# Optimization experiments

Measured on AMD Instinct MI355X. Metric: run time of the kernel, lower is better.

The kernel has to match this reference:

```python
import jax, jax.numpy as jnp
import numpy as np

C = 32
H = 8

def _layernorm(x, scale, bias, eps=1e-5):
    mu = jnp.mean(x, axis=-1, keepdims=True)
    var = jnp.mean(jnp.square(x - mu), axis=-1, keepdims=True)
    return (x - mu) * jax.lax.rsqrt(var + eps) * scale + bias


def setup_inputs() -> dict:
    key = jax.random.key(0)
    ks = jax.random.split(key, 10)
    B, s, i, j = 1, 128, 256, 256
    m = jax.random.normal(ks[0], (B, s, i, C), dtype=jnp.float32)
    z = jax.random.normal(ks[1], (B, i, j, C), dtype=jnp.float32)
    sd = 1.0 / np.sqrt(C)
    return {
        "m": m,
        "z": z,
        "ln_scale": jnp.ones((C,), jnp.float32),
        "ln_bias": jnp.zeros((C,), jnp.float32),
        "lnb_scale": jnp.ones((C,), jnp.float32),
        "lnb_bias": jnp.zeros((C,), jnp.float32),
        "wq": jax.random.normal(ks[2], (C, C * H), jnp.float32) * sd,
        "wk": jax.random.normal(ks[3], (C, C * H), jnp.float32) * sd,
        "wv": jax.random.normal(ks[4], (C, C * H), jnp.float32) * sd,
        "wb": jax.random.normal(ks[5], (C, H), jnp.float32) * sd,
        "wg": jax.random.normal(ks[6], (C, C * H), jnp.float32) * sd,
        "wo": jax.random.normal(ks[7], (C * H, C), jnp.float32) * (1.0 / np.sqrt(C * H)),
        "bo": jnp.zeros((C,), jnp.float32),
    }


def reference(m, z, ln_scale, ln_bias, lnb_scale, lnb_bias, wq, wk, wv, wb, wg, wo, bo):
    B, s, i, _ = m.shape
    j = z.shape[2]
    mn = _layernorm(m, ln_scale, ln_bias)                      # (B,s,i,c)
    q = (mn @ wq).reshape(B, s, i, H, C)                        # (B,s,i,h,c)
    k = (mn @ wk).reshape(B, s, i, H, C)
    v = (mn @ wv).reshape(B, s, i, H, C)
    gate = jax.nn.sigmoid(mn @ wg).reshape(B, s, i, H, C)       # (B,s,i,h,c)
    b = (_layernorm(z, lnb_scale, lnb_bias) @ wb)               # (B,i,j,h)
    a = jnp.einsum('bsihc,bsjhc->bsijh', q, k) * (C ** -0.5) + b[:, None]
    a = jax.nn.softmax(a, axis=-2)                              # softmax over j
    o = gate * jnp.einsum('bsijh,bsjhc->bsihc', a, v)
    o = o.reshape(B, s, i, H * C)
    return o @ wo + bo
```

## Files before the change

### kernel.cpp

```cpp
#include <hip/hip_runtime.h>

constexpr int NC = 32;
constexpr int NH = 8;
constexpr int NS = 128;
constexpr int NI = 256;
constexpr int NJ = 256;
constexpr float LN_EPS = 1e-5f;
constexpr float QSCALE = 0.17677669529663687f;
constexpr float LOG2E  = 1.4426950408889634f;

typedef __bf16 bf16x8 __attribute__((ext_vector_type(8)));
typedef __bf16 bf16x2 __attribute__((ext_vector_type(2)));
typedef float floatx4 __attribute__((ext_vector_type(4)));

__device__ __forceinline__ float fexp2(float x) {
#if __has_builtin(__builtin_amdgcn_exp2f)
    return __builtin_amdgcn_exp2f(x);
#else
    return exp2f(x);
#endif
}
__device__ __forceinline__ float frcp(float x) {
#if __has_builtin(__builtin_amdgcn_rcpf)
    return __builtin_amdgcn_rcpf(x);
#else
    return 1.0f / x;
#endif
}
__device__ __forceinline__ unsigned pk2c(float a, float b) {
    union { bf16x2 v; unsigned u; } c;
    c.v = bf16x2{(__bf16)a, (__bf16)b};
    return c.u;
}
__device__ __forceinline__ unsigned pkbb(__bf16 a, __bf16 b) {
    union { bf16x2 v; unsigned u; } c;
    c.v = bf16x2{a, b};
    return c.u;
}

__global__ __launch_bounds__(256) void biasprep_kernel(
    const float* __restrict__ z, const float* __restrict__ lnb_s,
    const float* __restrict__ lnb_b, const float* __restrict__ wb,
    const float* __restrict__ wq, const float* __restrict__ wk,
    const float* __restrict__ wv, const float* __restrict__ wg,
    const float* __restrict__ wo,
    float* __restrict__ bias32, unsigned short* __restrict__ wprep,
    unsigned short* __restrict__ wofrag)
{
    const int b = blockIdx.x;
    const int t = threadIdx.x;
    if (b < 256) {
        __shared__ float zL[256 * 33];
        const float4* src = (const float4*)(z + (size_t)b * NJ * NC);
#pragma unroll
        for (int k = 0; k < 8; ++k) {
            int idx = t + 256 * k;
            float4 v = src[idx];
            int f = idx * 4;
            int j = f >> 5, c = f & 31;
            zL[j * 33 + c]     = v.x; zL[j * 33 + c + 1] = v.y;
            zL[j * 33 + c + 2] = v.z; zL[j * 33 + c + 3] = v.w;
        }
        __syncthreads();

        float x[NC];
#pragma unroll
        for (int c = 0; c < NC; ++c) x[c] = zL[t * 33 + c];
        float mu = 0.f;
#pragma unroll
        for (int c = 0; c < NC; ++c) mu += x[c];
        mu *= (1.0f / NC);
        float var = 0.f;
#pragma unroll
        for (int c = 0; c < NC; ++c) { float d = x[c] - mu; var += d * d; }
        var *= (1.0f / NC);
        float rs = rsqrtf(var + LN_EPS);
        float acc[NH];
#pragma unroll
        for (int h = 0; h < NH; ++h) acc[h] = 0.f;
#pragma unroll
        for (int c = 0; c < NC; ++c) {
            float xn = (x[c] - mu) * rs * lnb_s[c] + lnb_b[c];
#pragma unroll
            for (int h = 0; h < NH; ++h) acc[h] += xn * wb[c * NH + h];
        }
        const int i = b;
        const int w_ = i >> 6, it = (i >> 4) & 3, lm = i & 15;
        const int jc = t >> 5, jt = (t >> 4) & 1, lq = (t >> 2) & 3, r = t & 3;
        const int base = jc * 8192 + w_ * 2048 + (jt * 4 + it) * 256
                       + (lq * 16 + lm) * 4 + r;
#pragma unroll
        for (int h = 0; h < NH; ++h)
            bias32[h * 65536 + base] = acc[h] * LOG2E;
    } else if (b < 272) {
        int g = (b - 256) * 256 + t;
        int p  = g >> 10;
        int h  = (g >> 7) & 7;
        int ct = (g >> 6) & 1;
        int l  = g & 63;
        const float* W = (p == 0) ? wq : (p == 1) ? wk : (p == 2) ? wv : wg;
        float scale = (p == 0) ? QSCALE * LOG2E : (p == 3) ? LOG2E : 1.0f;
        int col = 32 * h + 16 * ct + (l & 15);
        int r0  = 8 * (l >> 4);
        float v[8];
#pragma unroll
        for (int e = 0; e < 8; ++e) v[e] = W[(r0 + e) * 256 + col] * scale;
        uint4 u;
        u.x = pk2c(v[0], v[1]); u.y = pk2c(v[2], v[3]);
        u.z = pk2c(v[4], v[5]); u.w = pk2c(v[6], v[7]);
        *(uint4*)&wprep[g * 8] = u;
    } else {
        int g = (b - 272) * 256 + t;
        int tile = g >> 6;
        int l = g & 63;
        int kt = tile >> 1, nt = tile & 1;
        int r0 = kt * 32 + 8 * (l >> 4);
        int col = nt * 16 + (l & 15);
        float v[8];
#pragma unroll
        for (int e = 0; e < 8; ++e) v[e] = wo[(r0 + e) * 32 + col];
        uint4 u;
        u.x = pk2c(v[0], v[1]); u.y = pk2c(v[2], v[3]);
        u.z = pk2c(v[4], v[5]); u.w = pk2c(v[6], v[7]);
        *(uint4*)&wofrag[g * 8] = u;
    }
}

__global__ __launch_bounds__(256, 2) void attn_kernel(
    const float* __restrict__ m, const float* __restrict__ ln_s,
    const float* __restrict__ ln_b,
    const unsigned short* __restrict__ wprep,
    const float* __restrict__ bias32,
    unsigned short* __restrict__ attn16)
{
    __shared__ unsigned short QPX[256 * 40];
    __shared__ unsigned short Kt[256 * 40];
    __shared__ unsigned short Vt2[32 * 272];

    const int t = threadIdx.x;
    const int h = blockIdx.x & 7;
    const int s = blockIdx.x >> 3;
    const int l = t & 63, w = t >> 6;
    const int lm = l & 15, lq = l >> 4;
    const int ibase = w * 64;
    const floatx4 zero = {0.f, 0.f, 0.f, 0.f};

    {
        const float4* mr = (const float4*)(m + ((size_t)s * NI + t) * NC);
        float x[NC];
#pragma unroll
        for (int k = 0; k < 8; ++k) {
            float4 v = mr[k];
            x[4*k] = v.x; x[4*k+1] = v.y; x[4*k+2] = v.z; x[4*k+3] = v.w;
        }
        float mu = 0.f;
#pragma unroll
        for (int c = 0; c < NC; ++c) mu += x[c];
        mu *= (1.0f / NC);
        float var = 0.f;
#pragma unroll
        for (int c = 0; c < NC; ++c) { float d = x[c] - mu; var += d * d; }
        var *= (1.0f / NC);
        float rs = rsqrtf(var + LN_EPS);
#pragma unroll
        for (int k = 0; k < 4; ++k) {
            uint4 u;
            u.x = pk2c((x[8*k+0]-mu)*rs*ln_s[8*k+0]+ln_b[8*k+0],
                       (x[8*k+1]-mu)*rs*ln_s[8*k+1]+ln_b[8*k+1]);
            u.y = pk2c((x[8*k+2]-mu)*rs*ln_s[8*k+2]+ln_b[8*k+2],
                       (x[8*k+3]-mu)*rs*ln_s[8*k+3]+ln_b[8*k+3]);
            u.z = pk2c((x[8*k+4]-mu)*rs*ln_s[8*k+4]+ln_b[8*k+4],
                       (x[8*k+5]-mu)*rs*ln_s[8*k+5]+ln_b[8*k+5]);
            u.w = pk2c((x[8*k+6]-mu)*rs*ln_s[8*k+6]+ln_b[8*k+6],
                       (x[8*k+7]-mu)*rs*ln_s[8*k+7]+ln_b[8*k+7]);
            *(uint4*)&QPX[t * 40 + 8 * k] = u;
        }
    }

    const unsigned short* wp = wprep + ((size_t)h * 128 + l) * 8;
    bf16x8 wfQ[2], wfK[2], wfV[2], wfG[2];
#pragma unroll
    for (int ct = 0; ct < 2; ++ct) {
        wfQ[ct] = *(const bf16x8*)&wp[(0 * 1024 + ct * 64) * 8];
        wfK[ct] = *(const bf16x8*)&wp[(1 * 1024 + ct * 64) * 8];
        wfV[ct] = *(const bf16x8*)&wp[(2 * 1024 + ct * 64) * 8];
        wfG[ct] = *(const bf16x8*)&wp[(3 * 1024 + ct * 64) * 8];
    }
    bf16x8 Xb[4];
#pragma unroll
    for (int it = 0; it < 4; ++it)
        Xb[it] = *(const bf16x8*)&QPX[(ibase + it * 16 + lm) * 40 + lq * 8];

#pragma unroll
    for (int it = 0; it < 4; ++it)
#pragma unroll
        for (int ct = 0; ct < 2; ++ct) {
            floatx4 d = __builtin_amdgcn_mfma_f32_16x16x32_bf16(wfQ[ct], Xb[it], zero, 0, 0, 0);
            uint2 u; u.x = pk2c(d[0], d[1]); u.y = pk2c(d[2], d[3]);
            *(uint2*)&QPX[(ibase + it * 16 + lm) * 40 + ct * 16 + lq * 4] = u;
        }
#pragma unroll
    for (int it = 0; it < 4; ++it)
#pragma unroll
        for (int ct = 0; ct < 2; ++ct) {
            floatx4 d = __builtin_amdgcn_mfma_f32_16x16x32_bf16(wfK[ct], Xb[it], zero, 0, 0, 0);
            uint2 u; u.x = pk2c(d[0], d[1]); u.y = pk2c(d[2], d[3]);
            *(uint2*)&Kt[(ibase + it * 16 + lm) * 40 + ct * 16 + lq * 4] = u;
        }
#pragma unroll
    for (int jt = 0; jt < 4; ++jt)
#pragma unroll
        for (int ct = 0; ct < 2; ++ct) {
            floatx4 d = __builtin_amdgcn_mfma_f32_16x16x32_bf16(Xb[jt], wfV[ct], zero, 0, 0, 0);
            uint2 u; u.x = pk2c(d[0], d[1]); u.y = pk2c(d[2], d[3]);
            *(uint2*)&Vt2[(ct * 16 + lm) * 272 + ibase + jt * 16 + lq * 4] = u;
        }
    float gt[2][4][4];
#pragma unroll
    for (int it = 0; it < 4; ++it)
#pragma unroll
        for (int ct = 0; ct < 2; ++ct) {
            floatx4 d = __builtin_amdgcn_mfma_f32_16x16x32_bf16(wfG[ct], Xb[it], zero, 0, 0, 0);
#pragma unroll
            for (int r = 0; r < 4; ++r)
                gt[ct][it][r] = frcp(1.0f + fexp2(-d[r]));
        }

    __syncthreads();

    bf16x8 Qb[4];
#pragma unroll
    for (int it = 0; it < 4; ++it)
        Qb[it] = *(const bf16x8*)&QPX[(ibase + it * 16 + lm) * 40 + lq * 8];

    floatx4 accO[2][4];
#pragma unroll
    for (int ct = 0; ct < 2; ++ct)
#pragma unroll
        for (int it = 0; it < 4; ++it) accO[ct][it] = zero;
    float lsum[4] = {0.f, 0.f, 0.f, 0.f};

    const float* bptr = bias32 + (size_t)h * 65536 + w * 2048 + l * 4;

    for (int jc = 0; jc < 8; ++jc) {
        const int j0 = jc * 32;
        const float* bj = bptr + jc * 8192;

        bf16x8 Ka0 = *(const bf16x8*)&Kt[(j0 + lm) * 40 + lq * 8];
        bf16x8 Ka1 = *(const bf16x8*)&Kt[(j0 + 16 + lm) * 40 + lq * 8];
        bf16x8 Va0 = *(const bf16x8*)&Vt2[lm * 272 + j0 + lq * 8];
        bf16x8 Va1 = *(const bf16x8*)&Vt2[(16 + lm) * 272 + j0 + lq * 8];

#pragma unroll
        for (int jt = 0; jt < 2; ++jt) {
            bf16x8 Ka = jt ? Ka1 : Ka0;
#pragma unroll
            for (int it = 0; it < 4; ++it) {
                floatx4 C = *(const floatx4*)(bj + (jt * 4 + it) * 256);
                floatx4 S = __builtin_amdgcn_mfma_f32_16x16x32_bf16(Ka, Qb[it], C, 0, 0, 0);
                __bf16 p0 = (__bf16)fexp2(S[0]);
                __bf16 p1 = (__bf16)fexp2(S[1]);
                __bf16 p2 = (__bf16)fexp2(S[2]);
                __bf16 p3 = (__bf16)fexp2(S[3]);
                lsum[it] += ((float)p0 + (float)p1) + ((float)p2 + (float)p3);
                uint2 u; u.x = pkbb(p0, p1); u.y = pkbb(p2, p3);
                *(uint2*)&QPX[(ibase + it * 16 + lm) * 40 + jt * 16 + lq * 4] = u;
            }
        }

#pragma unroll
        for (int it = 0; it < 4; ++it) {
            bf16x8 Pb = *(const bf16x8*)&QPX[(ibase + it * 16 + lm) * 40 + lq * 8];
            accO[0][it] = __builtin_amdgcn_mfma_f32_16x16x32_bf16(Va0, Pb, accO[0][it], 0, 0, 0);
            accO[1][it] = __builtin_amdgcn_mfma_f32_16x16x32_bf16(Va1, Pb, accO[1][it], 0, 0, 0);
        }
    }

    float inv[4];
#pragma unroll
    for (int it = 0; it < 4; ++it) {
        float v = lsum[it];
        v += __shfl_xor(v, 16, 64);
        v += __shfl_xor(v, 32, 64);
        inv[it] = frcp(v);
    }
#pragma unroll
    for (int it = 0; it < 4; ++it) {
        const size_t rowb = ((size_t)s * NI + ibase + it * 16 + lm) * 256 + h * 32;
#pragma unroll
        for (int ct = 0; ct < 2; ++ct) {
            float o0 = accO[ct][it][0] * inv[it] * gt[ct][it][0];
            float o1 = accO[ct][it][1] * inv[it] * gt[ct][it][1];
            float o2 = accO[ct][it][2] * inv[it] * gt[ct][it][2];
            float o3 = accO[ct][it][3] * inv[it] * gt[ct][it][3];
            uint2 u; u.x = pk2c(o0, o1); u.y = pk2c(o2, o3);
            *(uint2*)&attn16[rowb + ct * 16 + lq * 4] = u;
        }
    }
}

__global__ __launch_bounds__(256) void proj_kernel(
    const unsigned short* __restrict__ attn16,
    const unsigned short* __restrict__ wofrag,
    const float* __restrict__ bo, float* __restrict__ out)
{
    const int t = threadIdx.x;
    const int l = t & 63, w = t >> 6;
    const int lm = l & 15, lq = l >> 4;
    const int row0 = blockIdx.x * 128 + w * 32;
    const floatx4 zero = {0.f, 0.f, 0.f, 0.f};

    floatx4 acc[2][2];
#pragma unroll
    for (int it = 0; it < 2; ++it)
#pragma unroll
        for (int nt = 0; nt < 2; ++nt) acc[it][nt] = zero;

#pragma unroll 2
    for (int kt = 0; kt < 8; ++kt) {
        bf16x8 a0 = *(const bf16x8*)&attn16[(size_t)(row0 + lm) * 256 + kt * 32 + lq * 8];
        bf16x8 a1 = *(const bf16x8*)&attn16[(size_t)(row0 + 16 + lm) * 256 + kt * 32 + lq * 8];
        bf16x8 b0 = *(const bf16x8*)&wofrag[((kt * 2 + 0) * 64 + l) * 8];
        bf16x8 b1 = *(const bf16x8*)&wofrag[((kt * 2 + 1) * 64 + l) * 8];
        acc[0][0] = __builtin_amdgcn_mfma_f32_16x16x32_bf16(a0, b0, acc[0][0], 0, 0, 0);
        acc[0][1] = __builtin_amdgcn_mfma_f32_16x16x32_bf16(a0, b1, acc[0][1], 0, 0, 0);
        acc[1][0] = __builtin_amdgcn_mfma_f32_16x16x32_bf16(a1, b0, acc[1][0], 0, 0, 0);
        acc[1][1] = __builtin_amdgcn_mfma_f32_16x16x32_bf16(a1, b1, acc[1][1], 0, 0, 0);
    }

    float bov[2] = {bo[lm], bo[16 + lm]};
#pragma unroll
    for (int it = 0; it < 2; ++it)
#pragma unroll
        for (int nt = 0; nt < 2; ++nt)
#pragma unroll
            for (int r = 0; r < 4; ++r)
                out[(size_t)(row0 + it * 16 + lq * 4 + r) * NC + nt * 16 + lm]
                    = acc[it][nt][r] + bov[nt];
}

extern "C" void kernel_launch(void* const* d_in, const int* in_sizes, int n_in,
                              void* d_out, int out_size, void* d_ws, size_t ws_size,
                              hipStream_t stream) {
    const float* m     = (const float*)d_in[0];
    const float* z     = (const float*)d_in[1];
    const float* ln_s  = (const float*)d_in[2];
    const float* ln_b  = (const float*)d_in[3];
    const float* lnb_s = (const float*)d_in[4];
    const float* lnb_b = (const float*)d_in[5];
    const float* wq    = (const float*)d_in[6];
    const float* wk    = (const float*)d_in[7];
    const float* wv    = (const float*)d_in[8];
    const float* wb    = (const float*)d_in[9];
    const float* wg    = (const float*)d_in[10];
    const float* wo    = (const float*)d_in[11];
    const float* bo    = (const float*)d_in[12];
    float* out = (float*)d_out;

    float* bias32 = (float*)d_ws;
    unsigned short* wprep  = (unsigned short*)((char*)d_ws + (2u << 20));
    unsigned short* wofrag = (unsigned short*)((char*)d_ws + (2u << 20) + 65536);
    unsigned short* attn16 = (unsigned short*)((char*)d_ws + (2u << 20) + 65536 + 16384);

    biasprep_kernel<<<276, 256, 0, stream>>>(z, lnb_s, lnb_b, wb, wq, wk, wv, wg,
                                             wo, bias32, wprep, wofrag);
    attn_kernel<<<NS * NH, 256, 0, stream>>>(m, ln_s, ln_b, wprep, bias32, attn16);
    proj_kernel<<<(NS * NI) / 128, 256, 0, stream>>>(attn16, wofrag, bo, out);
}
```

Baseline: 127.4 us.

## Software-pipeline attention loop with double-buffered P and register-resident K

Restructures the per-chunk attention loop so the PV MFMAs for the previous chunk run after the QK/exp of the current chunk, using a second LDS buffer for P. It preloads all K fragments into registers, prefetches the next chunk's bias one iteration ahead, and defers the gate projection until after the loop to free registers during it. The aim is to hide LDS and global load latency and keep the MFMA unit busy. In exchange it raises register and LDS pressure, which may reduce occupancy under launch bounds of 2 blocks per SM.

```diff
diff --git a/kernel.cpp b/kernel.cpp
--- a/kernel.cpp
+++ b/kernel.cpp
@@ -134,6 +134,7 @@
     unsigned short* __restrict__ attn16)
 {
     __shared__ unsigned short QPX[256 * 40];
+    __shared__ unsigned short Pb1[256 * 40];
     __shared__ unsigned short Kt[256 * 40];
     __shared__ unsigned short Vt2[32 * 272];
 
@@ -178,13 +179,12 @@
     }
 
     const unsigned short* wp = wprep + ((size_t)h * 128 + l) * 8;
-    bf16x8 wfQ[2], wfK[2], wfV[2], wfG[2];
+    bf16x8 wfQ[2], wfK[2], wfV[2];
 #pragma unroll
     for (int ct = 0; ct < 2; ++ct) {
         wfQ[ct] = *(const bf16x8*)&wp[(0 * 1024 + ct * 64) * 8];
         wfK[ct] = *(const bf16x8*)&wp[(1 * 1024 + ct * 64) * 8];
         wfV[ct] = *(const bf16x8*)&wp[(2 * 1024 + ct * 64) * 8];
-        wfG[ct] = *(const bf16x8*)&wp[(3 * 1024 + ct * 64) * 8];
     }
     bf16x8 Xb[4];
 #pragma unroll
@@ -215,24 +215,21 @@
             uint2 u; u.x = pk2c(d[0], d[1]); u.y = pk2c(d[2], d[3]);
             *(uint2*)&Vt2[(ct * 16 + lm) * 272 + ibase + jt * 16 + lq * 4] = u;
         }
-    float gt[2][4][4];
-#pragma unroll
-    for (int it = 0; it < 4; ++it)
-#pragma unroll
-        for (int ct = 0; ct < 2; ++ct) {
-            floatx4 d = __builtin_amdgcn_mfma_f32_16x16x32_bf16(wfG[ct], Xb[it], zero, 0, 0, 0);
-#pragma unroll
-            for (int r = 0; r < 4; ++r)
-                gt[ct][it][r] = frcp(1.0f + fexp2(-d[r]));
-        }
-
-    __syncthreads();
 
     bf16x8 Qb[4];
 #pragma unroll
     for (int it = 0; it < 4; ++it)
         Qb[it] = *(const bf16x8*)&QPX[(ibase + it * 16 + lm) * 40 + lq * 8];
 
+    __syncthreads();
+
+    bf16x8 Kf[8][2];
+#pragma unroll
+    for (int jcx = 0; jcx < 8; ++jcx) {
+        Kf[jcx][0] = *(const bf16x8*)&Kt[(jcx * 32 + lm) * 40 + lq * 8];
+        Kf[jcx][1] = *(const bf16x8*)&Kt[(jcx * 32 + 16 + lm) * 40 + lq * 8];
+    }
+
     floatx4 accO[2][4];
 #pragma unroll
     for (int ct = 0; ct < 2; ++ct)
@@ -242,40 +239,88 @@
 
     const float* bptr = bias32 + (size_t)h * 65536 + w * 2048 + l * 4;
 
+    floatx4 Cb[8];
+#pragma unroll
+    for (int q = 0; q < 8; ++q) Cb[q] = *(const floatx4*)(bptr + q * 256);
+
+    bf16x8 Vp0, Vp1;
+
+#pragma unroll
     for (int jc = 0; jc < 8; ++jc) {
         const int j0 = jc * 32;
-        const float* bj = bptr + jc * 8192;
-
-        bf16x8 Ka0 = *(const bf16x8*)&Kt[(j0 + lm) * 40 + lq * 8];
-        bf16x8 Ka1 = *(const bf16x8*)&Kt[(j0 + 16 + lm) * 40 + lq * 8];
-        bf16x8 Va0 = *(const bf16x8*)&Vt2[lm * 272 + j0 + lq * 8];
-        bf16x8 Va1 = *(const bf16x8*)&Vt2[(16 + lm) * 272 + j0 + lq * 8];
-
-#pragma unroll
-        for (int jt = 0; jt < 2; ++jt) {
-            bf16x8 Ka = jt ? Ka1 : Ka0;
+        bf16x8 Vc0 = *(const bf16x8*)&Vt2[lm * 272 + j0 + lq * 8];
+        bf16x8 Vc1 = *(const bf16x8*)&Vt2[(16 + lm) * 272 + j0 + lq * 8];
+
+        floatx4 S[2][4];
+#pragma unroll
+        for (int jt = 0; jt < 2; ++jt)
+#pragma unroll
+            for (int it = 0; it < 4; ++it)
+                S[jt][it] = __builtin_amdgcn_mfma_f32_16x16x32_bf16(
+                    Kf[jc][jt], Qb[it], Cb[jt * 4 + it], 0, 0, 0);
+
+        if (jc < 7) {
+            const float* bn = bptr + (jc + 1) * 8192;
+#pragma unroll
+            for (int q = 0; q < 8; ++q) Cb[q] = *(const floatx4*)(bn + q * 256);
+        }
+
+        unsigned short* Pc = (jc & 1) ? Pb1 : QPX;
+        const unsigned short* Pp = (jc & 1) ? QPX : Pb1;
+
+        bf16x8 Pfrag[4];
+        if (jc > 0) {
+#pragma unroll
+            for (int it = 0; it < 4; ++it)
+                Pfrag[it] = *(const bf16x8*)&Pp[(ibase + it * 16 + lm) * 40 + lq * 8];
+        }
+
+#pragma unroll
+        for (int jt = 0; jt < 2; ++jt)
 #pragma unroll
             for (int it = 0; it < 4; ++it) {
-                floatx4 C = *(const floatx4*)(bj + (jt * 4 + it) * 256);
-                floatx4 S = __builtin_amdgcn_mfma_f32_16x16x32_bf16(Ka, Qb[it], C, 0, 0, 0);
-                __bf16 p0 = (__bf16)fexp2(S[0]);
-                __bf16 p1 = (__bf16)fexp2(S[1]);
-                __bf16 p2 = (__bf16)fexp2(S[2]);
-                __bf16 p3 = (__bf16)fexp2(S[3]);
+                __bf16 p0 = (__bf16)fexp2(S[jt][it][0]);
+                __bf16 p1 = (__bf16)fexp2(S[jt][it][1]);
+                __bf16 p2 = (__bf16)fexp2(S[jt][it][2]);
+                __bf16 p3 = (__bf16)fexp2(S[jt][it][3]);
                 lsum[it] += ((float)p0 + (float)p1) + ((float)p2 + (float)p3);
                 uint2 u; u.x = pkbb(p0, p1); u.y = pkbb(p2, p3);
-                *(uint2*)&QPX[(ibase + it * 16 + lm) * 40 + jt * 16 + lq * 4] = u;
+                *(uint2*)&Pc[(ibase + it * 16 + lm) * 40 + jt * 16 + lq * 4] = u;
             }
-        }
-
+
+        if (jc > 0) {
+#pragma unroll
+            for (int it = 0; it < 4; ++it) {
+                accO[0][it] = __builtin_amdgcn_mfma_f32_16x16x32_bf16(Vp0, Pfrag[it], accO[0][it], 0, 0, 0);
+                accO[1][it] = __builtin_amdgcn_mfma_f32_16x16x32_bf16(Vp1, Pfrag[it], accO[1][it], 0, 0, 0);
+            }
+        }
+        Vp0 = Vc0; Vp1 = Vc1;
+    }
+    {
 #pragma unroll
         for (int it = 0; it < 4; ++it) {
-            bf16x8 Pb = *(const bf16x8*)&QPX[(ibase + it * 16 + lm) * 40 + lq * 8];
-            accO[0][it] = __builtin_amdgcn_mfma_f32_16x16x32_bf16(Va0, Pb, accO[0][it], 0, 0, 0);
-            accO[1][it] = __builtin_amdgcn_mfma_f32_16x16x32_bf16(Va1, Pb, accO[1][it], 0, 0, 0);
-        }
-    }
-
+            bf16x8 Pfrag = *(const bf16x8*)&Pb1[(ibase + it * 16 + lm) * 40 + lq * 8];
+            accO[0][it] = __builtin_amdgcn_mfma_f32_16x16x32_bf16(Vp0, Pfrag, accO[0][it], 0, 0, 0);
+            accO[1][it] = __builtin_amdgcn_mfma_f32_16x16x32_bf16(Vp1, Pfrag, accO[1][it], 0, 0, 0);
+        }
+    }
+
+    float gt[2][4][4];
+    {
+        bf16x8 wfG0 = *(const bf16x8*)&wp[(3 * 1024 + 0 * 64) * 8];
+        bf16x8 wfG1 = *(const bf16x8*)&wp[(3 * 1024 + 1 * 64) * 8];
+#pragma unroll
+        for (int it = 0; it < 4; ++it) {
+            floatx4 d0 = __builtin_amdgcn_mfma_f32_16x16x32_bf16(wfG0, Xb[it], zero, 0, 0, 0);
+            floatx4 d1 = __builtin_amdgcn_mfma_f32_16x16x32_bf16(wfG1, Xb[it], zero, 0, 0, 0);
+#pragma unroll
+            for (int r = 0; r < 4; ++r) {
+                gt[0][it][r] = frcp(1.0f + fexp2(-d0[r]));
+                gt[1][it][r] = frcp(1.0f + fexp2(-d1[r]));
+            }
+        }
+    }
     float inv[4];
 #pragma unroll
     for (int it = 0; it < 4; ++it) {
```

Result: slower. 178.4 us (+40.0%).

## Swizzle attention LDS layout, defer gate GEMM, and compute row sums via MFMA

Applied to the files above, without the earlier changes.

Replaces the padded LDS tiles (stride 40/272) with unpadded XOR-swizzled layouts for Q/P, K and V, shrinking shared memory so the launch bound can request 3 blocks per SIMD group instead of 2. The sigmoid gate projection moves from before the attention loop to after it, so its registers are not live during the loop. Softmax denominators are accumulated with an extra MFMA against a ones vector instead of scalar adds plus cross-lane shuffles. K and V fragments are now loaded inside the loop rather than hoisted, which trades register pressure for more LDS reads and extra MFMA work per chunk.

```diff
diff --git a/kernel.cpp b/kernel.cpp
--- a/kernel.cpp
+++ b/kernel.cpp
@@ -36,6 +36,13 @@
     union { bf16x2 v; unsigned u; } c;
     c.v = bf16x2{a, b};
     return c.u;
+}
+
+__device__ __forceinline__ int qkOff(int row, int chunk) {
+    return row * 32 + ((chunk ^ ((row >> 1) & 3)) << 3);
+}
+__device__ __forceinline__ int vOff(int c, int chunk) {
+    return c * 256 + ((chunk ^ (c & 7)) << 3);
 }
 
 __global__ __launch_bounds__(256) void biasprep_kernel(
@@ -126,16 +133,16 @@
     }
 }
 
-__global__ __launch_bounds__(256, 2) void attn_kernel(
+__global__ __launch_bounds__(256, 3) void attn_kernel(
     const float* __restrict__ m, const float* __restrict__ ln_s,
     const float* __restrict__ ln_b,
     const unsigned short* __restrict__ wprep,
     const float* __restrict__ bias32,
     unsigned short* __restrict__ attn16)
 {
-    __shared__ unsigned short QPX[256 * 40];
-    __shared__ unsigned short Kt[256 * 40];
-    __shared__ unsigned short Vt2[32 * 272];
+    __shared__ unsigned short QPX[256 * 32];
+    __shared__ unsigned short Kt[256 * 32];
+    __shared__ unsigned short Vt[32 * 256];
 
     const int t = threadIdx.x;
     const int h = blockIdx.x & 7;
@@ -173,23 +180,22 @@
                        (x[8*k+5]-mu)*rs*ln_s[8*k+5]+ln_b[8*k+5]);
             u.w = pk2c((x[8*k+6]-mu)*rs*ln_s[8*k+6]+ln_b[8*k+6],
                        (x[8*k+7]-mu)*rs*ln_s[8*k+7]+ln_b[8*k+7]);
-            *(uint4*)&QPX[t * 40 + 8 * k] = u;
+            *(uint4*)&QPX[qkOff(t, k)] = u;
         }
     }
 
     const unsigned short* wp = wprep + ((size_t)h * 128 + l) * 8;
-    bf16x8 wfQ[2], wfK[2], wfV[2], wfG[2];
+    bf16x8 wfQ[2], wfK[2], wfV[2];
 #pragma unroll
     for (int ct = 0; ct < 2; ++ct) {
         wfQ[ct] = *(const bf16x8*)&wp[(0 * 1024 + ct * 64) * 8];
         wfK[ct] = *(const bf16x8*)&wp[(1 * 1024 + ct * 64) * 8];
         wfV[ct] = *(const bf16x8*)&wp[(2 * 1024 + ct * 64) * 8];
-        wfG[ct] = *(const bf16x8*)&wp[(3 * 1024 + ct * 64) * 8];
     }
     bf16x8 Xb[4];
 #pragma unroll
     for (int it = 0; it < 4; ++it)
-        Xb[it] = *(const bf16x8*)&QPX[(ibase + it * 16 + lm) * 40 + lq * 8];
+        Xb[it] = *(const bf16x8*)&QPX[qkOff(ibase + it * 16 + lm, lq)];
 
 #pragma unroll
     for (int it = 0; it < 4; ++it)
@@ -197,7 +203,8 @@
         for (int ct = 0; ct < 2; ++ct) {
             floatx4 d = __builtin_amdgcn_mfma_f32_16x16x32_bf16(wfQ[ct], Xb[it], zero, 0, 0, 0);
             uint2 u; u.x = pk2c(d[0], d[1]); u.y = pk2c(d[2], d[3]);
-            *(uint2*)&QPX[(ibase + it * 16 + lm) * 40 + ct * 16 + lq * 4] = u;
+            int row = ibase + it * 16 + lm;
+            *(uint2*)&QPX[qkOff(row, 2 * ct + (lq >> 1)) + (lq & 1) * 4] = u;
         }
 #pragma unroll
     for (int it = 0; it < 4; ++it)
@@ -205,7 +212,8 @@
         for (int ct = 0; ct < 2; ++ct) {
             floatx4 d = __builtin_amdgcn_mfma_f32_16x16x32_bf16(wfK[ct], Xb[it], zero, 0, 0, 0);
             uint2 u; u.x = pk2c(d[0], d[1]); u.y = pk2c(d[2], d[3]);
-            *(uint2*)&Kt[(ibase + it * 16 + lm) * 40 + ct * 16 + lq * 4] = u;
+            int row = ibase + it * 16 + lm;
+            *(uint2*)&Kt[qkOff(row, 2 * ct + (lq >> 1)) + (lq & 1) * 4] = u;
         }
 #pragma unroll
     for (int jt = 0; jt < 4; ++jt)
@@ -213,32 +221,29 @@
         for (int ct = 0; ct < 2; ++ct) {
             floatx4 d = __builtin_amdgcn_mfma_f32_16x16x32_bf16(Xb[jt], wfV[ct], zero, 0, 0, 0);
             uint2 u; u.x = pk2c(d[0], d[1]); u.y = pk2c(d[2], d[3]);
-            *(uint2*)&Vt2[(ct * 16 + lm) * 272 + ibase + jt * 16 + lq * 4] = u;
-        }
-    float gt[2][4][4];
+            int c = ct * 16 + lm;
+            int chunk = 8 * w + 2 * jt + (lq >> 1);
+            *(uint2*)&Vt[vOff(c, chunk) + (lq & 1) * 4] = u;
+        }
+
+    bf16x8 Qb[4];
 #pragma unroll
     for (int it = 0; it < 4; ++it)
-#pragma unroll
-        for (int ct = 0; ct < 2; ++ct) {
-            floatx4 d = __builtin_amdgcn_mfma_f32_16x16x32_bf16(wfG[ct], Xb[it], zero, 0, 0, 0);
-#pragma unroll
-            for (int r = 0; r < 4; ++r)
-                gt[ct][it][r] = frcp(1.0f + fexp2(-d[r]));
-        }
+        Qb[it] = *(const bf16x8*)&QPX[qkOff(ibase + it * 16 + lm, lq)];
 
     __syncthreads();
 
-    bf16x8 Qb[4];
-#pragma unroll
-    for (int it = 0; it < 4; ++it)
-        Qb[it] = *(const bf16x8*)&QPX[(ibase + it * 16 + lm) * 40 + lq * 8];
-
     floatx4 accO[2][4];
 #pragma unroll
     for (int ct = 0; ct < 2; ++ct)
 #pragma unroll
         for (int it = 0; it < 4; ++it) accO[ct][it] = zero;
-    float lsum[4] = {0.f, 0.f, 0.f, 0.f};
+    floatx4 accL[4];
+#pragma unroll
+    for (int it = 0; it < 4; ++it) accL[it] = zero;
+    bf16x8 ones;
+#pragma unroll
+    for (int e = 0; e < 8; ++e) ones[e] = (__bf16)1.0f;
 
     const float* bptr = bias32 + (size_t)h * 65536 + w * 2048 + l * 4;
 
@@ -246,14 +251,9 @@
         const int j0 = jc * 32;
         const float* bj = bptr + jc * 8192;
 
-        bf16x8 Ka0 = *(const bf16x8*)&Kt[(j0 + lm) * 40 + lq * 8];
-        bf16x8 Ka1 = *(const bf16x8*)&Kt[(j0 + 16 + lm) * 40 + lq * 8];
-        bf16x8 Va0 = *(const bf16x8*)&Vt2[lm * 272 + j0 + lq * 8];
-        bf16x8 Va1 = *(const bf16x8*)&Vt2[(16 + lm) * 272 + j0 + lq * 8];
-
 #pragma unroll
         for (int jt = 0; jt < 2; ++jt) {
-            bf16x8 Ka = jt ? Ka1 : Ka0;
+            bf16x8 Ka = *(const bf16x8*)&Kt[qkOff(j0 + jt * 16 + lm, lq)];
 #pragma unroll
             for (int it = 0; it < 4; ++it) {
                 floatx4 C = *(const floatx4*)(bj + (jt * 4 + it) * 256);
@@ -262,37 +262,48 @@
                 __bf16 p1 = (__bf16)fexp2(S[1]);
                 __bf16 p2 = (__bf16)fexp2(S[2]);
                 __bf16 p3 = (__bf16)fexp2(S[3]);
-                lsum[it] += ((float)p0 + (float)p1) + ((float)p2 + (float)p3);
                 uint2 u; u.x = pkbb(p0, p1); u.y = pkbb(p2, p3);
-                *(uint2*)&QPX[(ibase + it * 16 + lm) * 40 + jt * 16 + lq * 4] = u;
+                int row = ibase + it * 16 + lm;
+                *(uint2*)&QPX[qkOff(row, 2 * jt + (lq >> 1)) + (lq & 1) * 4] = u;
             }
         }
 
+        bf16x8 Va0 = *(const bf16x8*)&Vt[vOff(lm, 4 * jc + lq)];
+        bf16x8 Va1 = *(const bf16x8*)&Vt[vOff(16 + lm, 4 * jc + lq)];
 #pragma unroll
         for (int it = 0; it < 4; ++it) {
-            bf16x8 Pb = *(const bf16x8*)&QPX[(ibase + it * 16 + lm) * 40 + lq * 8];
+            bf16x8 Pb = *(const bf16x8*)&QPX[qkOff(ibase + it * 16 + lm, lq)];
             accO[0][it] = __builtin_amdgcn_mfma_f32_16x16x32_bf16(Va0, Pb, accO[0][it], 0, 0, 0);
             accO[1][it] = __builtin_amdgcn_mfma_f32_16x16x32_bf16(Va1, Pb, accO[1][it], 0, 0, 0);
-        }
-    }
-
-    float inv[4];
+            accL[it]    = __builtin_amdgcn_mfma_f32_16x16x32_bf16(ones, Pb, accL[it], 0, 0, 0);
+        }
+    }
+
+    float gt[2][4][4];
+    {
+        bf16x8 wfG0 = *(const bf16x8*)&wp[(3 * 1024 + 0 * 64) * 8];
+        bf16x8 wfG1 = *(const bf16x8*)&wp[(3 * 1024 + 1 * 64) * 8];
+#pragma unroll
+        for (int it = 0; it < 4; ++it) {
+            floatx4 d0 = __builtin_amdgcn_mfma_f32_16x16x32_bf16(wfG0, Xb[it], zero, 0, 0, 0);
+            floatx4 d1 = __builtin_amdgcn_mfma_f32_16x16x32_bf16(wfG1, Xb[it], zero, 0, 0, 0);
+#pragma unroll
+            for (int r = 0; r < 4; ++r) {
+                gt[0][it][r] = frcp(1.0f + fexp2(-d0[r]));
+                gt[1][it][r] = frcp(1.0f + fexp2(-d1[r]));
+            }
+        }
+    }
 #pragma unroll
     for (int it = 0; it < 4; ++it) {
-        float v = lsum[it];
-        v += __shfl_xor(v, 16, 64);
-        v += __shfl_xor(v, 32, 64);
-        inv[it] = frcp(v);
-    }
-#pragma unroll
-    for (int it = 0; it < 4; ++it) {
+        const float inv = frcp(accL[it][0]);
         const size_t rowb = ((size_t)s * NI + ibase + it * 16 + lm) * 256 + h * 32;
 #pragma unroll
         for (int ct = 0; ct < 2; ++ct) {
-            float o0 = accO[ct][it][0] * inv[it] * gt[ct][it][0];
-            float o1 = accO[ct][it][1] * inv[it] * gt[ct][it][1];
-            float o2 = accO[ct][it][2] * inv[it] * gt[ct][it][2];
-            float o3 = accO[ct][it][3] * inv[it] * gt[ct][it][3];
+            float o0 = accO[ct][it][0] * inv * gt[ct][it][0];
+            float o1 = accO[ct][it][1] * inv * gt[ct][it][1];
+            float o2 = accO[ct][it][2] * inv * gt[ct][it][2];
+            float o3 = accO[ct][it][3] * inv * gt[ct][it][3];
             uint2 u; u.x = pk2c(o0, o1); u.y = pk2c(o2, o3);
             *(uint2*)&attn16[rowb + ct * 16 + lq * 4] = u;
         }
```

After: 120.2 us. 5.7% less time.
